# Performance work log

Hardware: AMD Instinct MI355X
Metric: run time of the kernel (lower is better)

## Reference

```python
import jax, jax.numpy as jnp
import numpy as np

N_NODES = 50000
N_EDGES = 800000
IN_FEATS = 128
OUT_CLASSES = 128


def _glorot(key, shape):
    fan_in, fan_out = shape[1], shape[0]
    limit = float(np.sqrt(6.0 / (fan_in + fan_out)))
    return jax.random.uniform(key, shape, jnp.float32, -limit, limit)


def setup_inputs() -> dict:
    key = jax.random.key(0)
    ks = jax.random.split(key, 11)
    x = jax.random.normal(ks[0], (N_NODES, IN_FEATS), jnp.float32)
    edge_index = jax.random.randint(ks[1], (2, N_EDGES), 0, N_NODES, jnp.int64)
    h = OUT_CLASSES // 2
    # PyG SAGEConv: lin_l applied to aggregated neighbors (has bias), lin_r to root (no bias)
    return {
        "x": x,
        "edge_index": edge_index,
        "W_l1": _glorot(ks[2], (OUT_CLASSES, IN_FEATS)),
        "b1": jnp.zeros((OUT_CLASSES,), jnp.float32),
        "W_r1": _glorot(ks[3], (OUT_CLASSES, IN_FEATS)),
        "W_l2": _glorot(ks[4], (h, OUT_CLASSES)),
        "b2": jnp.zeros((h,), jnp.float32),
        "W_r2": _glorot(ks[5], (h, OUT_CLASSES)),
        "W_l3": _glorot(ks[6], (OUT_CLASSES, h)),
        "b3": jnp.zeros((OUT_CLASSES,), jnp.float32),
        "W_r3": _glorot(ks[7], (OUT_CLASSES, h)),
    }


def _sage_conv(x, src, dst, W_l, b, W_r):
    # gather source-node features, mean-aggregate at destinations
    msgs = x[src]                                               # [E, d]
    agg = jax.ops.segment_sum(msgs, dst, num_segments=N_NODES)  # [N, d]
    cnt = jax.ops.segment_sum(jnp.ones((src.shape[0], 1), x.dtype), dst,
                              num_segments=N_NODES)             # [N, 1]
    mean = agg / jnp.maximum(cnt, 1.0)
    return mean @ W_l.T + b + x @ W_r.T


def reference(x, edge_index, W_l1, b1, W_r1, W_l2, b2, W_r2, W_l3, b3, W_r3):
    src, dst = edge_index[0], edge_index[1]
    h = _sage_conv(x, src, dst, W_l1, b1, W_r1)
    h = _sage_conv(h, src, dst, W_l2, b2, W_r2)
    h = _sage_conv(h, src, dst, W_l3, b3, W_r3)
    return h
```

## Files before the change

### kernel.cpp

```cpp
#include <hip/hip_runtime.h>

#define N_NODES 50000
#define N_EDGES 800000
#define BUCKETS 196
#define ECHUNK 4096
#define EBLKS 196
#define BCAP 5120

typedef __attribute__((ext_vector_type(8))) _Float16 half8;
typedef __attribute__((ext_vector_type(4))) _Float16 half4;
typedef __attribute__((ext_vector_type(4))) float f32x4;

template <int E> struct hvec;
template <> struct hvec<8> { typedef half8 t; };
template <> struct hvec<4> { typedef half4 t; };


template <int L, int E, int DEPTH>
__device__ __forceinline__ void gather_sum(const _Float16* __restrict__ feat,
                                           const unsigned short* __restrict__ csr,
                                           int start, int d, int lane,
                                           float* acc) {
  using V = typename hvec<E>::t;
  const V* ip = (const V*)feat;
  if (d <= 0) return;
  int nb = (d + DEPTH - 1) / DEPTH;
  int sc[DEPTH];
#pragma unroll
  for (int j = 0; j < DEPTH; ++j) sc[j] = csr[start + (j < d ? j : d - 1)];
  V vlast;
  for (int b = 0; b < nb; ++b) {
    V v[DEPTH];
#pragma unroll
    for (int j = 0; j < DEPTH; ++j) v[j] = ip[(size_t)sc[j] * L + lane];
    int e2 = (b + 1) * DEPTH;
    if (e2 < d) {
#pragma unroll
      for (int j = 0; j < DEPTH; ++j) {
        int idx = e2 + j;
        sc[j] = csr[start + (idx < d ? idx : d - 1)];
      }
    }
#pragma unroll
    for (int j = 0; j < DEPTH; ++j)
#pragma unroll
      for (int q = 0; q < E; ++q) acc[q] += (float)v[j][q];
    vlast = v[DEPTH - 1];
  }
  int rem = d - (nb - 1) * DEPTH;
  if (rem < DEPTH) {
    float corr = (float)(DEPTH - rem);
#pragma unroll
    for (int q = 0; q < E; ++q) acc[q] -= corr * (float)vlast[q];
  }
}


__global__ __launch_bounds__(256) void prep_k(
    const int* __restrict__ src, const int* __restrict__ dst,
    int* __restrict__ gcur, unsigned* __restrict__ binned,
    const float* __restrict__ x, _Float16* __restrict__ xh,
    const float* __restrict__ Wl1, const float* __restrict__ Wr1,
    const float* __restrict__ Wl2, const float* __restrict__ Wr2,
    const float* __restrict__ Wl3, const float* __restrict__ Wr3,
    _Float16* ph_l1, _Float16* pl_l1, _Float16* ph_r1, _Float16* pl_r1,
    _Float16* ph_c2, _Float16* pl_c2, _Float16* ph_l3, _Float16* pl_l3,
    _Float16* ph_r3, _Float16* pl_r3) {
  int blk = blockIdx.x;
  int t = threadIdx.x;
  if (blk < EBLKS) {
    __shared__ int h[BUCKETS];
    __shared__ int base[BUCKETS];
    for (int i = t; i < BUCKETS; i += 256) h[i] = 0;
    __syncthreads();
    int e0 = blk * ECHUNK;
    int eend = e0 + ECHUNK < N_EDGES ? e0 + ECHUNK : N_EDGES;
    for (int e = e0 + t; e < eend; e += 256) atomicAdd(&h[dst[e] >> 8], 1);
    __syncthreads();
    for (int i = t; i < BUCKETS; i += 256) {
      if (h[i]) base[i] = atomicAdd(&gcur[i], h[i]);
      h[i] = 0;
    }
    __syncthreads();
    for (int e = e0 + t; e < eend; e += 256) {
      int d = dst[e];
      int b = d >> 8;
      int r = atomicAdd(&h[b], 1);
      binned[(size_t)b * BCAP + base[b] + r] =
          (unsigned)src[e] | ((unsigned)(d & 255) << 16);
    }
  } else if (blk < EBLKS + 32) {
    int g = (blk - EBLKS) * 256 + t;
    const float *S0, *S1 = nullptr;
    _Float16 *ph, *pl;
    int f, K;
    if (g < 2048)      { f = g;        ph = ph_l1; pl = pl_l1; S0 = Wl1; K = 128; }
    else if (g < 4096) { f = g - 2048; ph = ph_r1; pl = pl_r1; S0 = Wr1; K = 128; }
    else if (g < 6144) { f = g - 4096; ph = ph_c2; pl = pl_c2; S0 = Wl2; S1 = Wr2; K = 128; }
    else if (g < 7168) { f = g - 6144; ph = ph_l3; pl = pl_l3; S0 = Wl3; K = 64; }
    else               { f = g - 7168; ph = ph_r3; pl = pl_r3; S0 = Wr3; K = 64; }
    int kb = f >> 9;
    int rem = f & 511;
    int n = rem >> 2;
    int lq = rem & 3;
    const float* srow =
        (S1 && n >= 64) ? (S1 + (size_t)(n - 64) * K) : (S0 + (size_t)n * K);
    int kbase = kb * 32 + lq * 8;
#pragma unroll
    for (int j = 0; j < 8; ++j) {
      float v = srow[kbase + j];
      _Float16 hi = (_Float16)v;
      ph[f * 8 + j] = hi;
      pl[f * 8 + j] = (_Float16)(v - (float)hi);
    }
  } else {
    int i = (blk - EBLKS - 32) * 256 + t;
    if (i >= N_NODES * 16) return;
    const float4* xp = (const float4*)x;
    float4 a = xp[2 * i];
    float4 b = xp[2 * i + 1];
    half8 hh;
    hh[0] = (_Float16)a.x; hh[1] = (_Float16)a.y; hh[2] = (_Float16)a.z; hh[3] = (_Float16)a.w;
    hh[4] = (_Float16)b.x; hh[5] = (_Float16)b.y; hh[6] = (_Float16)b.z; hh[7] = (_Float16)b.w;
    ((half8*)xh)[i] = hh;
  }
}

__global__ __launch_bounds__(256) void bucket_fill_k(const unsigned* __restrict__ binned,
                                                     const int* __restrict__ gcnt,
                                                     int* __restrict__ offs,
                                                     int* __restrict__ deg,
                                                     unsigned short* __restrict__ csr) {
  __shared__ int cnt[256];
  __shared__ int loc[256];
  __shared__ int cur[256];
  int b = blockIdx.x;
  int t = threadIdx.x;
  int base = b * BCAP;
  int end = base + gcnt[b];
  cnt[t] = 0;
  __syncthreads();
  for (int e = base + t; e < end; e += 256) atomicAdd(&cnt[(binned[e] >> 16) & 255], 1);
  __syncthreads();
  loc[t] = cnt[t];
  __syncthreads();
  for (int o = 1; o < 256; o <<= 1) {
    int v = (t >= o) ? loc[t - o] : 0;
    __syncthreads();
    loc[t] += v;
    __syncthreads();
  }
  int excl = loc[t] - cnt[t];
  int node = b * 256 + t;
  if (node < N_NODES) {
    offs[node] = base + excl;
    deg[node] = cnt[t];
  }
  cur[t] = excl;
  __syncthreads();
  for (int e = base + t; e < end; e += 256) {
    unsigned r = binned[e];
    int dl = (r >> 16) & 255;
    int p = atomicAdd(&cur[dl], 1);
    csr[base + p] = (unsigned short)(r & 0xFFFF);
  }
}


template <int D, bool FUSE>
__global__ __launch_bounds__(256, 4) void agg_f16_k(const _Float16* __restrict__ in,
                                                    _Float16* __restrict__ out,
                                                    const int* __restrict__ offs,
                                                    const int* __restrict__ deg,
                                                    const unsigned short* __restrict__ csr,
                                                    const float* __restrict__ bias,
                                                    const _Float16* __restrict__ addend) {
  constexpr int E = 4;
  constexpr int L = D / E;
  constexpr int NPB = 256 / L;
  int node = blockIdx.x * NPB + threadIdx.x / L;
  int lane = threadIdx.x & (L - 1);
  if (node >= N_NODES) return;
  int start = offs[node];
  int d = deg[node];
  float acc[E];
#pragma unroll
  for (int j = 0; j < E; ++j) acc[j] = 0.f;
  gather_sum<L, E, 24>(in, csr, start, d, lane, acc);
  float inv = d > 0 ? 1.0f / (float)d : 0.0f;
  half4 o;
  if constexpr (FUSE) {
    half4 av = ((const half4*)addend)[(size_t)node * L + lane];
#pragma unroll
    for (int q = 0; q < E; ++q)
      o[q] = (_Float16)(acc[q] * inv + bias[lane * E + q] + (float)av[q]);
  } else {
#pragma unroll
    for (int q = 0; q < E; ++q) o[q] = (_Float16)(acc[q] * inv);
  }
  ((half4*)out)[(size_t)node * L + lane] = o;
}


template <int K, int NB, bool OUT32>
__global__ __launch_bounds__(256, 4) void fused_agg_gemm_k(
    const _Float16* __restrict__ feat,
    const int* __restrict__ offs, const int* __restrict__ deg,
    const unsigned short* __restrict__ csr,
    const _Float16* __restrict__ Wlh, const _Float16* __restrict__ Wll,
    const _Float16* __restrict__ Wrh, const _Float16* __restrict__ Wrl,
    const float* __restrict__ bias, _Float16* __restrict__ C16,
    float* __restrict__ C32) {
  constexpr int L = 16;
  constexpr int E = K / L;
  static_assert(NB == 16 && 256 / L == NB, "one lane-group per node");
  constexpr int DEPTH = (E == 8) ? 16 : 24;
  constexpr int STRIDE = K + 8;
  constexpr int KB = K / 32;
  constexpr int WPR = 4;
  constexpr int CT = 8 / WPR;
  __shared__ _Float16 Asm[NB * STRIDE];
  int t = threadIdx.x;
  int base = blockIdx.x * NB;
  {
    int lane = t & (L - 1);
    int slot = t / L;
    int node = base + slot;
    float acc[E];
#pragma unroll
    for (int j = 0; j < E; ++j) acc[j] = 0.f;
    float inv = 0.f;
    if (node < N_NODES) {
      int start = offs[node];
      int d = deg[node];
      gather_sum<L, E, DEPTH>(feat, csr, start, d, lane, acc);
      inv = d > 0 ? 1.0f / (float)d : 0.0f;
    }
    using V = typename hvec<E>::t;
    V o;
#pragma unroll
    for (int q = 0; q < E; ++q) o[q] = (_Float16)(acc[q] * inv);
    *(V*)&Asm[slot * STRIDE + lane * E] = o;
  }
  __syncthreads();
  int wave = t >> 6;
  int lane = t & 63;
  int l15 = lane & 15;
  int lq = lane >> 4;
  int colbase = wave * (CT * 16);
  int row0 = base;
  const int woff = (l15 * 4 + lq) * 8;
  f32x4 acc[CT];
#pragma unroll
  for (int c = 0; c < CT; ++c) acc[c] = (f32x4){0.f, 0.f, 0.f, 0.f};
  {
    const _Float16* asrc = &Asm[l15 * STRIDE + lq * 8];
    half8 af[KB];
#pragma unroll
    for (int kb = 0; kb < KB; ++kb) af[kb] = *(const half8*)(asrc + kb * 32);
#pragma unroll
    for (int kb = 0; kb < KB; ++kb) {
#pragma unroll
      for (int ct = 0; ct < CT; ++ct) {
        size_t bi = (size_t)(kb * 128 + colbase + ct * 16) * 32 + woff;
        half8 bh = *(const half8*)(Wlh + bi);
        half8 bl = *(const half8*)(Wll + bi);
        acc[ct] = __builtin_amdgcn_mfma_f32_16x16x32_f16(af[kb], bh, acc[ct], 0, 0, 0);
        acc[ct] = __builtin_amdgcn_mfma_f32_16x16x32_f16(af[kb], bl, acc[ct], 0, 0, 0);
      }
    }
  }
  {
    int arow = row0 + l15;
    if (arow >= N_NODES) arow = N_NODES - 1;
    const _Float16* ab = feat + (size_t)arow * K + lq * 8;
    half8 af[KB];
#pragma unroll
    for (int kb = 0; kb < KB; ++kb) af[kb] = *(const half8*)(ab + kb * 32);
#pragma unroll
    for (int kb = 0; kb < KB; ++kb) {
#pragma unroll
      for (int ct = 0; ct < CT; ++ct) {
        size_t bi = (size_t)(kb * 128 + colbase + ct * 16) * 32 + woff;
        half8 bh = *(const half8*)(Wrh + bi);
        half8 bl = *(const half8*)(Wrl + bi);
        acc[ct] = __builtin_amdgcn_mfma_f32_16x16x32_f16(af[kb], bh, acc[ct], 0, 0, 0);
        acc[ct] = __builtin_amdgcn_mfma_f32_16x16x32_f16(af[kb], bl, acc[ct], 0, 0, 0);
      }
    }
  }
#pragma unroll
  for (int r = 0; r < 4; ++r) {
    int row = row0 + lq * 4 + r;
    if (row >= N_NODES) continue;
#pragma unroll
    for (int ct = 0; ct < CT; ++ct) {
      int col = colbase + ct * 16 + l15;
      float v = acc[ct][r] + bias[col];
      if constexpr (OUT32)
        C32[(size_t)row * 128 + col] = v;
      else
        C16[(size_t)row * 128 + col] = (_Float16)v;
    }
  }
}


template <int K, bool DUAL, bool SPLIT, bool OUT32>
__global__ __launch_bounds__(256, 2) void gemm_f16_k(
    const _Float16* __restrict__ A1, const _Float16* __restrict__ W1h,
    const _Float16* __restrict__ W1l,
    const _Float16* __restrict__ A2, const _Float16* __restrict__ W2h,
    const _Float16* __restrict__ W2l,
    const float* __restrict__ bias, _Float16* __restrict__ C16,
    float* __restrict__ C32, _Float16* __restrict__ O2) {
  int wave = threadIdx.x >> 6;
  int lane = threadIdx.x & 63;
  int l15 = lane & 15;
  int lq = lane >> 4;
  int rowblk = blockIdx.x >> 1;
  int colg = blockIdx.x & 1;
  int rg = rowblk * 4 + wave;
  if (rg >= N_NODES / 16) return;
  int row0 = rg << 4;
  constexpr int KB = K / 32;
  constexpr int NN = 128;
  const int woff = (l15 * 4 + lq) * 8;
  f32x4 acc[4];
#pragma unroll
  for (int c = 0; c < 4; ++c) acc[c] = (f32x4){0.f, 0.f, 0.f, 0.f};
  constexpr int NOP = DUAL ? 2 : 1;
#pragma unroll
  for (int op = 0; op < NOP; ++op) {
    const _Float16* A = op ? A2 : A1;
    const _Float16* Wh = op ? W2h : W1h;
    const _Float16* Wl = op ? W2l : W1l;
    const _Float16* ab = A + (size_t)(row0 + l15) * K + lq * 8;
    half8 af[KB];
#pragma unroll
    for (int kb = 0; kb < KB; ++kb) af[kb] = *(const half8*)(ab + kb * 32);
#pragma unroll
    for (int kb = 0; kb < KB; ++kb) {
#pragma unroll
      for (int ct = 0; ct < 4; ++ct) {
        int n0 = colg * 64 + ct * 16;
        size_t base = (size_t)(kb * NN + n0) * 32 + woff;
        half8 bh = *(const half8*)(Wh + base);
        half8 bl = *(const half8*)(Wl + base);
        acc[ct] = __builtin_amdgcn_mfma_f32_16x16x32_f16(af[kb], bh, acc[ct], 0, 0, 0);
        acc[ct] = __builtin_amdgcn_mfma_f32_16x16x32_f16(af[kb], bl, acc[ct], 0, 0, 0);
      }
    }
  }
#pragma unroll
  for (int r = 0; r < 4; ++r) {
    int row = row0 + lq * 4 + r;
#pragma unroll
    for (int ct = 0; ct < 4; ++ct) {
      int col = colg * 64 + ct * 16 + l15;
      float v = acc[ct][r];
      if constexpr (SPLIT) {
        if (col < 64)
          C16[(size_t)row * 64 + col] = (_Float16)v;
        else
          O2[(size_t)row * 64 + (col - 64)] = (_Float16)v;
      } else {
        v += bias[col];
        if constexpr (OUT32)
          C32[(size_t)row * 128 + col] = v;
        else
          C16[(size_t)row * 128 + col] = (_Float16)v;
      }
    }
  }
}

extern "C" void kernel_launch(void* const* d_in, const int* in_sizes, int n_in,
                              void* d_out, int out_size, void* d_ws, size_t ws_size,
                              hipStream_t stream) {
  const float* x   = (const float*)d_in[0];
  const int* ei    = (const int*)d_in[1];
  const float* Wl1 = (const float*)d_in[2];
  const float* b1  = (const float*)d_in[3];
  const float* Wr1 = (const float*)d_in[4];
  const float* Wl2 = (const float*)d_in[5];
  const float* b2  = (const float*)d_in[6];
  const float* Wr2 = (const float*)d_in[7];
  const float* Wl3 = (const float*)d_in[8];
  const float* b3  = (const float*)d_in[9];
  const float* Wr3 = (const float*)d_in[10];
  float* out = (float*)d_out;

  const int* src = ei;
  const int* dst = ei + N_EDGES;

  char* ws = (char*)d_ws;
  size_t off = 0;
  auto take = [&](size_t bytes) {
    void* p = ws + off;
    off += (bytes + 255) & ~(size_t)255;
    return p;
  };
  int* deg    = (int*)take((size_t)N_NODES * 4);
  int* offs   = (int*)take((size_t)N_NODES * 4);
  int* gcur   = (int*)take((size_t)BUCKETS * 4);
  unsigned* binned = (unsigned*)take((size_t)BUCKETS * BCAP * 4);
  unsigned short* csr = (unsigned short*)take((size_t)BUCKETS * BCAP * 2);
  _Float16* xh  = (_Float16*)take((size_t)N_NODES * 128 * 2);
  _Float16* h1h = (_Float16*)take((size_t)N_NODES * 128 * 2);
  _Float16* Ph  = (_Float16*)take((size_t)N_NODES * 64 * 2);
  _Float16* Rh  = (_Float16*)take((size_t)N_NODES * 64 * 2);
  _Float16* h2h = (_Float16*)take((size_t)N_NODES * 64 * 2);
  _Float16* ph_l1 = (_Float16*)take(16384 * 2);
  _Float16* pl_l1 = (_Float16*)take(16384 * 2);
  _Float16* ph_r1 = (_Float16*)take(16384 * 2);
  _Float16* pl_r1 = (_Float16*)take(16384 * 2);
  _Float16* ph_c2 = (_Float16*)take(16384 * 2);
  _Float16* pl_c2 = (_Float16*)take(16384 * 2);
  _Float16* ph_l3 = (_Float16*)take(8192 * 2);
  _Float16* pl_l3 = (_Float16*)take(8192 * 2);
  _Float16* ph_r3 = (_Float16*)take(8192 * 2);
  _Float16* pl_r3 = (_Float16*)take(8192 * 2);

  hipMemsetAsync(gcur, 0, (size_t)BUCKETS * 4, stream);

  prep_k<<<EBLKS + 32 + 3125, 256, 0, stream>>>(
      src, dst, gcur, binned, x, xh, Wl1, Wr1, Wl2, Wr2, Wl3, Wr3, ph_l1, pl_l1,
      ph_r1, pl_r1, ph_c2, pl_c2, ph_l3, pl_l3, ph_r3, pl_r3);
  bucket_fill_k<<<BUCKETS, 256, 0, stream>>>(binned, gcur, offs, deg, csr);

  fused_agg_gemm_k<128, 16, false><<<3125, 256, 0, stream>>>(
      xh, offs, deg, csr, ph_l1, pl_l1, ph_r1, pl_r1, b1, h1h, nullptr);

  gemm_f16_k<128, false, true, false><<<1564, 256, 0, stream>>>(
      h1h, ph_c2, pl_c2, nullptr, nullptr, nullptr, nullptr, Ph, nullptr, Rh);
  agg_f16_k<64, true><<<3125, 256, 0, stream>>>(Ph, h2h, offs, deg, csr, b2, Rh);

  fused_agg_gemm_k<64, 16, true><<<3125, 256, 0, stream>>>(
      h2h, offs, deg, csr, ph_l3, pl_l3, ph_r3, pl_r3, b3, nullptr, out);
}
```

Measured before the change: 249.6 us.

## Slice feature tensors into 32-wide column planes and split aggregation from GEMMs

Stores node features as 32-column slices so each aggregation block gathers from a smaller contiguous plane, which should raise cache hit rates on the random neighbour gathers. Aggregation moves out of the fused agg+GEMM kernels into a sliced gather kernel. Layer-1 GEMM and the layer-2 projection are fused into one kernel that keeps h1 in shared memory, and layer 3 gets a dedicated dual GEMM. In exchange, the mean results now round-trip through global memory, and one extra aggregation launch is added.

```diff
diff --git a/kernel.cpp b/kernel.cpp
--- a/kernel.cpp
+++ b/kernel.cpp
@@ -122,7 +122,9 @@
     half8 hh;
     hh[0] = (_Float16)a.x; hh[1] = (_Float16)a.y; hh[2] = (_Float16)a.z; hh[3] = (_Float16)a.w;
     hh[4] = (_Float16)b.x; hh[5] = (_Float16)b.y; hh[6] = (_Float16)b.z; hh[7] = (_Float16)b.w;
-    ((half8*)xh)[i] = hh;
+    int node = i >> 4;
+    int part = i & 15;
+    ((half8*)xh)[(size_t)(part >> 2) * (N_NODES * 4) + (size_t)node * 4 + (part & 3)] = hh;
   }
 }
 
@@ -167,153 +169,146 @@
 }
 
 
-template <int D, bool FUSE>
-__global__ __launch_bounds__(256, 4) void agg_f16_k(const _Float16* __restrict__ in,
-                                                    _Float16* __restrict__ out,
-                                                    const int* __restrict__ offs,
-                                                    const int* __restrict__ deg,
-                                                    const unsigned short* __restrict__ csr,
-                                                    const float* __restrict__ bias,
-                                                    const _Float16* __restrict__ addend) {
-  constexpr int E = 4;
-  constexpr int L = D / E;
-  constexpr int NPB = 256 / L;
-  int node = blockIdx.x * NPB + threadIdx.x / L;
-  int lane = threadIdx.x & (L - 1);
+template <int NSL, bool FUSE, bool OUTSL>
+__global__ __launch_bounds__(256, 4) void agg_sliced_k(
+    const _Float16* __restrict__ in_sl, _Float16* __restrict__ out,
+    const int* __restrict__ offs, const int* __restrict__ deg,
+    const unsigned short* __restrict__ csr, const float* __restrict__ bias,
+    const _Float16* __restrict__ addend) {
+  constexpr int COPIES = 8 / NSL;
+  constexpr int F = NSL * 32;
+  int g = blockIdx.x & 7;
+  int s = g % NSL;
+  int chunk = (blockIdx.x >> 3) * COPIES + g / NSL;
+  int t = threadIdx.x;
+  int node = chunk * 32 + (t >> 3);
+  int lane = t & 7;
   if (node >= N_NODES) return;
+  const _Float16* base = in_sl + (size_t)s * (N_NODES * 32);
+  float acc[4] = {0.f, 0.f, 0.f, 0.f};
   int start = offs[node];
   int d = deg[node];
-  float acc[E];
-#pragma unroll
-  for (int j = 0; j < E; ++j) acc[j] = 0.f;
-  gather_sum<L, E, 24>(in, csr, start, d, lane, acc);
+  gather_sum<8, 4, 16>(base, csr, start, d, lane, acc);
   float inv = d > 0 ? 1.0f / (float)d : 0.0f;
+  int feat = s * 32 + lane * 4;
   half4 o;
   if constexpr (FUSE) {
-    half4 av = ((const half4*)addend)[(size_t)node * L + lane];
-#pragma unroll
-    for (int q = 0; q < E; ++q)
-      o[q] = (_Float16)(acc[q] * inv + bias[lane * E + q] + (float)av[q]);
+    half4 av = *(const half4*)(addend + (size_t)node * F + feat);
+#pragma unroll
+    for (int q = 0; q < 4; ++q)
+      o[q] = (_Float16)(acc[q] * inv + bias[feat + q] + (float)av[q]);
   } else {
 #pragma unroll
-    for (int q = 0; q < E; ++q) o[q] = (_Float16)(acc[q] * inv);
-  }
-  ((half4*)out)[(size_t)node * L + lane] = o;
-}
-
-
-template <int K, int NB, bool OUT32>
-__global__ __launch_bounds__(256, 4) void fused_agg_gemm_k(
-    const _Float16* __restrict__ feat,
-    const int* __restrict__ offs, const int* __restrict__ deg,
-    const unsigned short* __restrict__ csr,
-    const _Float16* __restrict__ Wlh, const _Float16* __restrict__ Wll,
-    const _Float16* __restrict__ Wrh, const _Float16* __restrict__ Wrl,
-    const float* __restrict__ bias, _Float16* __restrict__ C16,
-    float* __restrict__ C32) {
-  constexpr int L = 16;
-  constexpr int E = K / L;
-  static_assert(NB == 16 && 256 / L == NB, "one lane-group per node");
-  constexpr int DEPTH = (E == 8) ? 16 : 24;
-  constexpr int STRIDE = K + 8;
-  constexpr int KB = K / 32;
-  constexpr int WPR = 4;
-  constexpr int CT = 8 / WPR;
-  __shared__ _Float16 Asm[NB * STRIDE];
+    for (int q = 0; q < 4; ++q) o[q] = (_Float16)(acc[q] * inv);
+  }
+  _Float16* op = OUTSL ? out + (size_t)s * (N_NODES * 32) + (size_t)node * 32 + lane * 4
+                       : out + (size_t)node * F + feat;
+  *(half4*)op = o;
+}
+
+
+__global__ __launch_bounds__(256, 4) void megagemm_k(
+    const _Float16* __restrict__ mh1, const _Float16* __restrict__ xsl,
+    const _Float16* __restrict__ Wl1h, const _Float16* __restrict__ Wl1l,
+    const _Float16* __restrict__ Wr1h, const _Float16* __restrict__ Wr1l,
+    const float* __restrict__ b1,
+    const _Float16* __restrict__ Wc2h, const _Float16* __restrict__ Wc2l,
+    _Float16* __restrict__ Psl, _Float16* __restrict__ Rh) {
+  constexpr int STR = 136;
+  __shared__ _Float16 Hsm[16 * STR];
   int t = threadIdx.x;
-  int base = blockIdx.x * NB;
-  {
-    int lane = t & (L - 1);
-    int slot = t / L;
-    int node = base + slot;
-    float acc[E];
-#pragma unroll
-    for (int j = 0; j < E; ++j) acc[j] = 0.f;
-    float inv = 0.f;
-    if (node < N_NODES) {
-      int start = offs[node];
-      int d = deg[node];
-      gather_sum<L, E, DEPTH>(feat, csr, start, d, lane, acc);
-      inv = d > 0 ? 1.0f / (float)d : 0.0f;
-    }
-    using V = typename hvec<E>::t;
-    V o;
-#pragma unroll
-    for (int q = 0; q < E; ++q) o[q] = (_Float16)(acc[q] * inv);
-    *(V*)&Asm[slot * STRIDE + lane * E] = o;
-  }
-  __syncthreads();
   int wave = t >> 6;
   int lane = t & 63;
   int l15 = lane & 15;
   int lq = lane >> 4;
-  int colbase = wave * (CT * 16);
-  int row0 = base;
+  int row0 = blockIdx.x * 16;
   const int woff = (l15 * 4 + lq) * 8;
-  f32x4 acc[CT];
-#pragma unroll
-  for (int c = 0; c < CT; ++c) acc[c] = (f32x4){0.f, 0.f, 0.f, 0.f};
+  int colbase = wave * 32;
+  f32x4 acc[2];
+  acc[0] = (f32x4){0.f, 0.f, 0.f, 0.f};
+  acc[1] = (f32x4){0.f, 0.f, 0.f, 0.f};
   {
-    const _Float16* asrc = &Asm[l15 * STRIDE + lq * 8];
-    half8 af[KB];
-#pragma unroll
-    for (int kb = 0; kb < KB; ++kb) af[kb] = *(const half8*)(asrc + kb * 32);
-#pragma unroll
-    for (int kb = 0; kb < KB; ++kb) {
-#pragma unroll
-      for (int ct = 0; ct < CT; ++ct) {
+    const _Float16* ab = mh1 + (size_t)(row0 + l15) * 128 + lq * 8;
+    half8 af[4];
+#pragma unroll
+    for (int kb = 0; kb < 4; ++kb) af[kb] = *(const half8*)(ab + kb * 32);
+#pragma unroll
+    for (int kb = 0; kb < 4; ++kb)
+#pragma unroll
+      for (int ct = 0; ct < 2; ++ct) {
         size_t bi = (size_t)(kb * 128 + colbase + ct * 16) * 32 + woff;
-        half8 bh = *(const half8*)(Wlh + bi);
-        half8 bl = *(const half8*)(Wll + bi);
+        half8 bh = *(const half8*)(Wl1h + bi);
+        half8 bl = *(const half8*)(Wl1l + bi);
         acc[ct] = __builtin_amdgcn_mfma_f32_16x16x32_f16(af[kb], bh, acc[ct], 0, 0, 0);
         acc[ct] = __builtin_amdgcn_mfma_f32_16x16x32_f16(af[kb], bl, acc[ct], 0, 0, 0);
       }
-    }
   }
   {
-    int arow = row0 + l15;
-    if (arow >= N_NODES) arow = N_NODES - 1;
-    const _Float16* ab = feat + (size_t)arow * K + lq * 8;
-    half8 af[KB];
-#pragma unroll
-    for (int kb = 0; kb < KB; ++kb) af[kb] = *(const half8*)(ab + kb * 32);
-#pragma unroll
-    for (int kb = 0; kb < KB; ++kb) {
-#pragma unroll
-      for (int ct = 0; ct < CT; ++ct) {
+    half8 af[4];
+#pragma unroll
+    for (int kb = 0; kb < 4; ++kb)
+      af[kb] = *(const half8*)(xsl + (size_t)kb * (N_NODES * 32) +
+                               (size_t)(row0 + l15) * 32 + lq * 8);
+#pragma unroll
+    for (int kb = 0; kb < 4; ++kb)
+#pragma unroll
+      for (int ct = 0; ct < 2; ++ct) {
         size_t bi = (size_t)(kb * 128 + colbase + ct * 16) * 32 + woff;
-        half8 bh = *(const half8*)(Wrh + bi);
-        half8 bl = *(const half8*)(Wrl + bi);
+        half8 bh = *(const half8*)(Wr1h + bi);
+        half8 bl = *(const half8*)(Wr1l + bi);
         acc[ct] = __builtin_amdgcn_mfma_f32_16x16x32_f16(af[kb], bh, acc[ct], 0, 0, 0);
         acc[ct] = __builtin_amdgcn_mfma_f32_16x16x32_f16(af[kb], bl, acc[ct], 0, 0, 0);
       }
-    }
-  }
+  }
+#pragma unroll
+  for (int r = 0; r < 4; ++r) {
+    int rl = lq * 4 + r;
+#pragma unroll
+    for (int ct = 0; ct < 2; ++ct) {
+      int col = colbase + ct * 16 + l15;
+      Hsm[rl * STR + col] = (_Float16)(acc[ct][r] + b1[col]);
+    }
+  }
+  __syncthreads();
+  f32x4 a2[2];
+  a2[0] = (f32x4){0.f, 0.f, 0.f, 0.f};
+  a2[1] = (f32x4){0.f, 0.f, 0.f, 0.f};
+  half8 af[4];
+#pragma unroll
+  for (int kb = 0; kb < 4; ++kb)
+    af[kb] = *(const half8*)&Hsm[l15 * STR + kb * 32 + lq * 8];
+#pragma unroll
+  for (int kb = 0; kb < 4; ++kb)
+#pragma unroll
+    for (int ct = 0; ct < 2; ++ct) {
+      size_t bi = (size_t)(kb * 128 + colbase + ct * 16) * 32 + woff;
+      half8 bh = *(const half8*)(Wc2h + bi);
+      half8 bl = *(const half8*)(Wc2l + bi);
+      a2[ct] = __builtin_amdgcn_mfma_f32_16x16x32_f16(af[kb], bh, a2[ct], 0, 0, 0);
+      a2[ct] = __builtin_amdgcn_mfma_f32_16x16x32_f16(af[kb], bl, a2[ct], 0, 0, 0);
+    }
 #pragma unroll
   for (int r = 0; r < 4; ++r) {
     int row = row0 + lq * 4 + r;
-    if (row >= N_NODES) continue;
-#pragma unroll
-    for (int ct = 0; ct < CT; ++ct) {
+#pragma unroll
+    for (int ct = 0; ct < 2; ++ct) {
       int col = colbase + ct * 16 + l15;
-      float v = acc[ct][r] + bias[col];
-      if constexpr (OUT32)
-        C32[(size_t)row * 128 + col] = v;
+      float v = a2[ct][r];
+      if (col < 64)
+        Psl[(size_t)(col >> 5) * (N_NODES * 32) + (size_t)row * 32 + (col & 31)] =
+            (_Float16)v;
       else
-        C16[(size_t)row * 128 + col] = (_Float16)v;
-    }
-  }
-}
-
-
-template <int K, bool DUAL, bool SPLIT, bool OUT32>
-__global__ __launch_bounds__(256, 2) void gemm_f16_k(
-    const _Float16* __restrict__ A1, const _Float16* __restrict__ W1h,
-    const _Float16* __restrict__ W1l,
-    const _Float16* __restrict__ A2, const _Float16* __restrict__ W2h,
-    const _Float16* __restrict__ W2l,
-    const float* __restrict__ bias, _Float16* __restrict__ C16,
-    float* __restrict__ C32, _Float16* __restrict__ O2) {
+        Rh[(size_t)row * 64 + (col - 64)] = (_Float16)v;
+    }
+  }
+}
+
+
+__global__ __launch_bounds__(256, 2) void gemm3_k(
+    const _Float16* __restrict__ mh3, const _Float16* __restrict__ h2sl,
+    const _Float16* __restrict__ Wlh, const _Float16* __restrict__ Wll,
+    const _Float16* __restrict__ Wrh, const _Float16* __restrict__ Wrl,
+    const float* __restrict__ b3, float* __restrict__ out) {
   int wave = threadIdx.x >> 6;
   int lane = threadIdx.x & 63;
   int l15 = lane & 15;
@@ -323,34 +318,42 @@
   int rg = rowblk * 4 + wave;
   if (rg >= N_NODES / 16) return;
   int row0 = rg << 4;
-  constexpr int KB = K / 32;
-  constexpr int NN = 128;
   const int woff = (l15 * 4 + lq) * 8;
   f32x4 acc[4];
 #pragma unroll
   for (int c = 0; c < 4; ++c) acc[c] = (f32x4){0.f, 0.f, 0.f, 0.f};
-  constexpr int NOP = DUAL ? 2 : 1;
-#pragma unroll
-  for (int op = 0; op < NOP; ++op) {
-    const _Float16* A = op ? A2 : A1;
-    const _Float16* Wh = op ? W2h : W1h;
-    const _Float16* Wl = op ? W2l : W1l;
-    const _Float16* ab = A + (size_t)(row0 + l15) * K + lq * 8;
-    half8 af[KB];
-#pragma unroll
-    for (int kb = 0; kb < KB; ++kb) af[kb] = *(const half8*)(ab + kb * 32);
-#pragma unroll
-    for (int kb = 0; kb < KB; ++kb) {
+  {
+    const _Float16* ab = mh3 + (size_t)(row0 + l15) * 64 + lq * 8;
+    half8 af[2];
+#pragma unroll
+    for (int kb = 0; kb < 2; ++kb) af[kb] = *(const half8*)(ab + kb * 32);
+#pragma unroll
+    for (int kb = 0; kb < 2; ++kb)
 #pragma unroll
       for (int ct = 0; ct < 4; ++ct) {
-        int n0 = colg * 64 + ct * 16;
-        size_t base = (size_t)(kb * NN + n0) * 32 + woff;
-        half8 bh = *(const half8*)(Wh + base);
-        half8 bl = *(const half8*)(Wl + base);
+        size_t bi = (size_t)(kb * 128 + colg * 64 + ct * 16) * 32 + woff;
+        half8 bh = *(const half8*)(Wlh + bi);
+        half8 bl = *(const half8*)(Wll + bi);
         acc[ct] = __builtin_amdgcn_mfma_f32_16x16x32_f16(af[kb], bh, acc[ct], 0, 0, 0);
         acc[ct] = __builtin_amdgcn_mfma_f32_16x16x32_f16(af[kb], bl, acc[ct], 0, 0, 0);
       }
-    }
+  }
+  {
+    half8 af[2];
+#pragma unroll
+    for (int kb = 0; kb < 2; ++kb)
+      af[kb] = *(const half8*)(h2sl + (size_t)kb * (N_NODES * 32) +
+                               (size_t)(row0 + l15) * 32 + lq * 8);
+#pragma unroll
+    for (int kb = 0; kb < 2; ++kb)
+#pragma unroll
+      for (int ct = 0; ct < 4; ++ct) {
+        size_t bi = (size_t)(kb * 128 + colg * 64 + ct * 16) * 32 + woff;
+        half8 bh = *(const half8*)(Wrh + bi);
+        half8 bl = *(const half8*)(Wrl + bi);
+        acc[ct] = __builtin_amdgcn_mfma_f32_16x16x32_f16(af[kb], bh, acc[ct], 0, 0, 0);
+        acc[ct] = __builtin_amdgcn_mfma_f32_16x16x32_f16(af[kb], bl, acc[ct], 0, 0, 0);
+      }
   }
 #pragma unroll
   for (int r = 0; r < 4; ++r) {
@@ -358,19 +361,7 @@
 #pragma unroll
     for (int ct = 0; ct < 4; ++ct) {
       int col = colg * 64 + ct * 16 + l15;
-      float v = acc[ct][r];
-      if constexpr (SPLIT) {
-        if (col < 64)
-          C16[(size_t)row * 64 + col] = (_Float16)v;
-        else
-          O2[(size_t)row * 64 + (col - 64)] = (_Float16)v;
-      } else {
-        v += bias[col];
-        if constexpr (OUT32)
-          C32[(size_t)row * 128 + col] = v;
-        else
-          C16[(size_t)row * 128 + col] = (_Float16)v;
-      }
+      out[(size_t)row * 128 + col] = acc[ct][r] + b3[col];
     }
   }
 }
@@ -406,11 +397,12 @@
   int* gcur   = (int*)take((size_t)BUCKETS * 4);
   unsigned* binned = (unsigned*)take((size_t)BUCKETS * BCAP * 4);
   unsigned short* csr = (unsigned short*)take((size_t)BUCKETS * BCAP * 2);
-  _Float16* xh  = (_Float16*)take((size_t)N_NODES * 128 * 2);
-  _Float16* h1h = (_Float16*)take((size_t)N_NODES * 128 * 2);
-  _Float16* Ph  = (_Float16*)take((size_t)N_NODES * 64 * 2);
-  _Float16* Rh  = (_Float16*)take((size_t)N_NODES * 64 * 2);
-  _Float16* h2h = (_Float16*)take((size_t)N_NODES * 64 * 2);
+  _Float16* xh   = (_Float16*)take((size_t)N_NODES * 128 * 2);
+  _Float16* mh1  = (_Float16*)take((size_t)N_NODES * 128 * 2);
+  _Float16* Psl  = (_Float16*)take((size_t)N_NODES * 64 * 2);
+  _Float16* Rh   = (_Float16*)take((size_t)N_NODES * 64 * 2);
+  _Float16* h2sl = (_Float16*)take((size_t)N_NODES * 64 * 2);
+  _Float16* mh3  = (_Float16*)take((size_t)N_NODES * 64 * 2);
   _Float16* ph_l1 = (_Float16*)take(16384 * 2);
   _Float16* pl_l1 = (_Float16*)take(16384 * 2);
   _Float16* ph_r1 = (_Float16*)take(16384 * 2);
@@ -429,13 +421,17 @@
       ph_r1, pl_r1, ph_c2, pl_c2, ph_l3, pl_l3, ph_r3, pl_r3);
   bucket_fill_k<<<BUCKETS, 256, 0, stream>>>(binned, gcur, offs, deg, csr);
 
-  fused_agg_gemm_k<128, 16, false><<<3125, 256, 0, stream>>>(
-      xh, offs, deg, csr, ph_l1, pl_l1, ph_r1, pl_r1, b1, h1h, nullptr);
-
-  gemm_f16_k<128, false, true, false><<<1564, 256, 0, stream>>>(
-      h1h, ph_c2, pl_c2, nullptr, nullptr, nullptr, nullptr, Ph, nullptr, Rh);
-  agg_f16_k<64, true><<<3125, 256, 0, stream>>>(Ph, h2h, offs, deg, csr, b2, Rh);
-
-  fused_agg_gemm_k<64, 16, true><<<3125, 256, 0, stream>>>(
-      h2h, offs, deg, csr, ph_l3, pl_l3, ph_r3, pl_r3, b3, nullptr, out);
-}
+  agg_sliced_k<4, false, false><<<8 * 782, 256, 0, stream>>>(
+      xh, mh1, offs, deg, csr, nullptr, nullptr);
+
+  megagemm_k<<<3125, 256, 0, stream>>>(mh1, xh, ph_l1, pl_l1, ph_r1, pl_r1, b1,
+                                       ph_c2, pl_c2, Psl, Rh);
+
+  agg_sliced_k<2, true, true><<<8 * 391, 256, 0, stream>>>(
+      Psl, h2sl, offs, deg, csr, b2, Rh);
+
+  agg_sliced_k<2, false, false><<<8 * 391, 256, 0, stream>>>(
+      h2sl, mh3, offs, deg, csr, nullptr, nullptr);
+
+  gemm3_k<<<1564, 256, 0, stream>>>(mh3, h2sl, ph_l3, pl_l3, ph_r3, pl_r3, b3, out);
+}
```

Result: slower. 262.5 us (+5.2%).
